# Optimization experiments

Measured on AMD Instinct MI355X. Metric: run time of the kernel, lower is better.

Reference implementation:

```python
import jax, jax.numpy as jnp
import numpy as np

B = 2048


def _maxpool2(x):
    return jax.lax.reduce_window(x, -jnp.inf, jax.lax.max,
                                 (1, 1, 2, 2), (1, 1, 2, 2), 'VALID')


def setup_inputs() -> dict:
    key = jax.random.key(0)
    ks = jax.random.split(key, 7)
    return {
        'x': jax.random.normal(ks[0], (B, 3, 32, 32), dtype=jnp.float32),
        'conv_w': jax.random.normal(ks[1], (45, 1, 5, 5), dtype=jnp.float32),
        'conv_b': jax.random.normal(ks[2], (45,), dtype=jnp.float32) * 0.1,
        'tree_w': jax.random.normal(ks[3], (1, 16, 15, 3, 7, 7, 2, 2), dtype=jnp.float32),
        'tree_b': jax.random.normal(ks[4], (1, 16, 3, 7), dtype=jnp.float32),
        'fc_w': jax.random.normal(ks[5], (10, 336), dtype=jnp.float32),
        'fc_b': jax.random.normal(ks[6], (10,), dtype=jnp.float32) * 0.1,
    }


def reference(x, conv_w, conv_b, tree_w, tree_b, fc_w, fc_b):
    # grouped conv: in=3, groups=3, out=45, kernel 5x5, VALID -> (B,45,28,28)
    out = jax.lax.conv_general_dilated(
        x, conv_w, window_strides=(1, 1), padding='VALID',
        dimension_numbers=('NCHW', 'OIHW', 'NCHW'), feature_group_count=3)
    out = jax.nn.sigmoid(out + conv_b[None, :, None, None])
    out = _maxpool2(out)  # (B,45,14,14)
    b = out.shape[0]
    # unfold((2,2),stride=2) + the torch reshape/transpose chain is equivalent to:
    # (B,45,14,14) -> (b, g=3, m=15, i=7, ki=2, j=7, kj=2) -> (b,m,g,i,j,ki,kj)
    xt = out.reshape(b, 3, 15, 7, 2, 7, 2).transpose(0, 2, 1, 3, 5, 4, 6)
    # TreeLayer: elementwise mul with weights (16,m,g,i,j,ki,kj) then sum over m,j,ki,kj
    t = jnp.einsum('bmgijkl,fmgijkl->bfgi', xt, tree_w[0]) + tree_b  # (B,16,3,7)
    t = jax.nn.sigmoid(t)
    return t.reshape(b, 16 * 3 * 7) @ fc_w.T + fc_b  # (B,10)
```

## Files before the change

kernel.cpp:

```cpp
#include <hip/hip_runtime.h>
#include <hip/hip_fp16.h>

#define BATCH 2048
#define NPREP 95

typedef _Float16 f16x8 __attribute__((ext_vector_type(8)));
typedef float f32x4 __attribute__((ext_vector_type(4)));

__device__ __forceinline__ float sigmoidf(float v) {
    return 1.0f / (1.0f + __expf(-v));
}

#define WS_W3B  0
#define WS_FCW  301056
#define WS_PS   322560
#define PS_G_STRIDE (7u * 2048u * 448u)

__global__ __launch_bounds__(256, 4) void kA_conv_prep(
    const float* __restrict__ x,
    const float* __restrict__ conv_w,
    const float* __restrict__ conv_b,
    const float* __restrict__ tree_w,
    const float* __restrict__ fc_w,
    ushort* __restrict__ W3B,
    float* __restrict__ FCW,
    ushort* __restrict__ ps3)
{
    __shared__ __align__(16) ushort xsc[3 * 4656];
    const int tid = threadIdx.x;

    if (blockIdx.x < NPREP) {
        int pidx = blockIdx.x * 256 + tid;
        if (pidx < 18816) {
            int gi = pidx / 896;
            int rem = pidx - gi * 896;
            int c = rem >> 6, lane2 = rem & 63;
            int f = lane2 & 15, qq = lane2 >> 4;
            int g = gi / 7, i = gi - g * 7;
            ushort h[8];
            #pragma unroll
            for (int u = 0; u < 8; u++) {
                int k = c * 32 + qq * 8 + u;
                int tt = k >> 6;
                int q2 = (k >> 4) & 3;
                int nn = k & 15;
                int u27 = tt * 4 + q2;
                int ki = u27 / 14;
                int pw = u27 - ki * 14;
                int j = pw >> 1, kj = pw & 1;
                float v = 0.f;
                if (nn < 15)
                    v = tree_w[(size_t)f * 8820 + nn * 588 + g * 196 + i * 28
                               + j * 4 + ki * 2 + kj];
                h[u] = __half_as_ushort(__float2half(v));
            }
            *(uint4*)(W3B + (size_t)pidx * 8) = *(uint4*)h;
        } else if (pidx < 24192) {
            int j = pidx - 18816;
            int f = j & 15, o = (j >> 4) & 15, gi = j >> 8;
            FCW[j] = (o < 10) ? fc_w[o * 336 + f * 21 + gi] : 0.f;
        }
        return;
    }

    const int img  = blockIdx.x - NPREP;
    const int lane = tid & 63;
    const int n    = lane & 15;
    const int q    = lane >> 4;
    const int wave = tid >> 6;

    const float4* xg = (const float4*)(x + (size_t)img * 3072);
    #pragma unroll
    for (int it = 0; it < 3; it++) {
        int idx = tid + it * 256;
        float4 v = xg[idx];
        int flat = idx * 4;
        int row = flat >> 5;
        int g = row >> 5, r = row & 31;
        int col = flat & 31;
        __half2 a = __float22half2_rn(make_float2(v.x, v.y));
        __half2 b = __float22half2_rn(make_float2(v.z, v.w));
        uint2 pk;
        pk.x = *(unsigned int*)&a;
        pk.y = *(unsigned int*)&b;
        *(uint2*)(xsc + g * 4656 + r * 36 + col) = pk;
    }
    if (tid < 96) {
        int g = tid >> 5, r = tid & 31;
        *(uint2*)(xsc + g * 4656 + r * 36 + 32) = make_uint2(0u, 0u);
    }

    f16x8 B1g[3], B2g[3];
    float biasg[3];
    #pragma unroll
    for (int g = 0; g < 3; g++) {
        f16x8 b1 = {0, 0, 0, 0, 0, 0, 0, 0};
        f16x8 b2 = {0, 0, 0, 0, 0, 0, 0, 0};
        float bb = 0.f;
        if (n < 15) {
            const float* wrow = conv_w + (g * 15 + n) * 25;
            #pragma unroll
            for (int u = 0; u < 5; u++) b1[u] = (_Float16)wrow[q * 5 + u];
            if (q == 0) {
                #pragma unroll
                for (int u = 0; u < 5; u++) b2[u] = (_Float16)wrow[20 + u];
            }
            bb = conv_b[g * 15 + n];
        }
        B1g[g] = b1; B2g[g] = b2; biasg[g] = bb;
    }
    __syncthreads();

    for (int t = tid; t < 2592; t += 256) {
        int gg = t / 864;
        int rem = t - gg * 864;
        int s = rem / 288 + 1;
        int rem2 = rem - (s - 1) * 288;
        int row = rem2 / 9, g4 = rem2 - row * 9;
        ushort* base = xsc + gg * 4656;
        ushort* dst = base + s * 1164 + row * 36 + g4 * 4;
        if (g4 == 8) { *(uint2*)dst = make_uint2(0u, 0u); continue; }
        uint2 lo = *(const uint2*)(base + row * 36 + g4 * 4);
        uint2 hi = *(const uint2*)(base + row * 36 + g4 * 4 + 4);
        unsigned int w0 = lo.x, w1 = lo.y, w2 = hi.x, w3 = hi.y;
        unsigned int o0, o1;
        if (s == 1)      { o0 = (w0 >> 16) | (w1 << 16); o1 = (w1 >> 16) | (w2 << 16); }
        else if (s == 2) { o0 = w1;                      o1 = w2; }
        else             { o0 = (w1 >> 16) | (w2 << 16); o1 = (w2 >> 16) | (w3 << 16); }
        *(uint2*)dst = make_uint2(o0, o1);
    }

    const int dr = (n >> 1) & 1, dc = n & 1, n4 = n >> 2;
    const int a2c = 144 - q * 36;
    int aoff[13], sv[13];
    #pragma unroll
    for (int it = 0; it < 13; it++) {
        int t = wave + it * 4;
        if (t < 49) {
            int pb = t * 4 + n4;
            int ph = pb / 14, pw = pb - ph * 14;
            int r = 2 * ph + dr, c = 2 * pw + dc;
            int s = c & 3;
            aoff[it] = s * 1164 + (r + q) * 36 + (c - s);
            int i = t / 7, tt = t - i * 7;
            sv[it] = (i * 2048 + img) * 448 + tt * 64 + lane;
        } else { aoff[it] = 0; sv[it] = 0; }
    }
    __syncthreads();

    #pragma unroll
    for (int g = 0; g < 3; g++) {
        const ushort* xb = xsc + g * 4656;
        const f16x8 B1 = B1g[g], B2 = B2g[g];
        const float bias = biasg[g];
        ushort* psg = ps3 + (size_t)g * PS_G_STRIDE;
        #pragma unroll
        for (int it = 0; it < 13; it++) {
            int t = wave + it * 4;
            if (t < 49) {
                const ushort* pA = xb + aoff[it];
                union { struct { uint2 a, b; } u; f16x8 v; } A1, A2;
                A1.u.a = *(const uint2*)pA;
                A1.u.b = *(const uint2*)(pA + 4);
                A2.u.a = *(const uint2*)(pA + a2c);
                A2.u.b = *(const uint2*)(pA + a2c + 4);
                f32x4 d = {0.f, 0.f, 0.f, 0.f};
                d = __builtin_amdgcn_mfma_f32_16x16x32_f16(A1.v, B1, d, 0, 0, 0);
                d = __builtin_amdgcn_mfma_f32_16x16x32_f16(A2.v, B2, d, 0, 0, 0);
                float mx = fmaxf(fmaxf(d[0], d[1]), fmaxf(d[2], d[3]));
                float val = (n < 15) ? sigmoidf(mx + bias) : 0.f;
                psg[sv[it]] = __half_as_ushort(__float2half(val));
            }
        }
    }
}

__global__ __launch_bounds__(128, 3) void kBC_tree_fc(
    const ushort* __restrict__ ps3,
    const ushort* __restrict__ W3B,
    const float* __restrict__ tree_b,
    const float* __restrict__ FCW,
    const float* __restrict__ fc_b,
    float* __restrict__ out)
{
    __shared__ __align__(16) ushort im[32 * 456];
    __shared__ __align__(16) ushort tsl[32 * 16];

    const int btile = blockIdx.x;
    const int gi    = blockIdx.y;
    const int img0  = btile * 32;
    const int tid   = threadIdx.x;
    const int lane  = tid & 63;
    const int n     = lane & 15;
    const int q     = lane >> 4;
    const int wave  = tid >> 6;

    const uint4* src = (const uint4*)(ps3 + ((size_t)gi * 2048 + img0) * 448);
    #pragma unroll
    for (int it = 0; it < 14; it++) {
        int t = tid + it * 128;
        int img = t / 56;
        int o = t - img * 56;
        *(uint4*)(im + img * 456 + o * 8) = src[t];
    }

    const f16x8* Wbase = (const f16x8*)W3B + (size_t)gi * 896;
    f16x8 B[14];
    #pragma unroll
    for (int c = 0; c < 14; c++) B[c] = Wbase[c * 64 + lane];
    __syncthreads();

    f32x4 D = {0.f, 0.f, 0.f, 0.f};
    const ushort* arow = im + (wave * 16 + n) * 456;
    #pragma unroll
    for (int c = 0; c < 14; c++) {
        f16x8 Af = *(const f16x8*)(arow + c * 32 + q * 8);
        D = __builtin_amdgcn_mfma_f32_16x16x32_f16(Af, B[c], D, 0, 0, 0);
    }

    float bias = tree_b[n * 21 + gi];
    #pragma unroll
    for (int r = 0; r < 4; r++) {
        int imgL = wave * 16 + q * 4 + r;
        tsl[imgL * 16 + n] = __half_as_ushort(__float2half(sigmoidf(D[r] + bias)));
    }
    __syncthreads();

    const float4* Wfc = (const float4*)(FCW + gi * 256);
    for (int t = tid; t < 320; t += 128) {
        int img = t / 10, o = t - (t / 10) * 10;
        const uint4* tp = (const uint4*)(tsl + img * 16);
        uint4 t0 = tp[0], t1 = tp[1];
        const __half2* h = (const __half2*)&t0;
        const __half2* h2 = (const __half2*)&t1;
        float4 w0 = Wfc[o * 4], w1 = Wfc[o * 4 + 1];
        float4 w2 = Wfc[o * 4 + 2], w3 = Wfc[o * 4 + 3];
        float acc = (gi == 0) ? fc_b[o] : 0.f;
        float2 p;
        p = __half22float2(h[0]);  acc = fmaf(p.x, w0.x, acc); acc = fmaf(p.y, w0.y, acc);
        p = __half22float2(h[1]);  acc = fmaf(p.x, w0.z, acc); acc = fmaf(p.y, w0.w, acc);
        p = __half22float2(h[2]);  acc = fmaf(p.x, w1.x, acc); acc = fmaf(p.y, w1.y, acc);
        p = __half22float2(h[3]);  acc = fmaf(p.x, w1.z, acc); acc = fmaf(p.y, w1.w, acc);
        p = __half22float2(h2[0]); acc = fmaf(p.x, w2.x, acc); acc = fmaf(p.y, w2.y, acc);
        p = __half22float2(h2[1]); acc = fmaf(p.x, w2.z, acc); acc = fmaf(p.y, w2.w, acc);
        p = __half22float2(h2[2]); acc = fmaf(p.x, w3.x, acc); acc = fmaf(p.y, w3.y, acc);
        p = __half22float2(h2[3]); acc = fmaf(p.x, w3.z, acc); acc = fmaf(p.y, w3.w, acc);
#if defined(__HIP_PLATFORM_AMD__)
        unsafeAtomicAdd(out + (size_t)(img0 + img) * 10 + o, acc);
#else
        atomicAdd(out + (size_t)(img0 + img) * 10 + o, acc);
#endif
    }
}

extern "C" void kernel_launch(void* const* d_in, const int* in_sizes, int n_in,
                              void* d_out, int out_size, void* d_ws, size_t ws_size,
                              hipStream_t stream) {
    const float* x      = (const float*)d_in[0];
    const float* conv_w = (const float*)d_in[1];
    const float* conv_b = (const float*)d_in[2];
    const float* tree_w = (const float*)d_in[3];
    const float* tree_b = (const float*)d_in[4];
    const float* fc_w   = (const float*)d_in[5];
    const float* fc_b   = (const float*)d_in[6];
    float* out = (float*)d_out;

    ushort* W3B = (ushort*)((char*)d_ws + WS_W3B);
    float*  FCW = (float*)((char*)d_ws + WS_FCW);
    ushort* ps3 = (ushort*)((char*)d_ws + WS_PS);

    hipMemsetAsync(out, 0, (size_t)BATCH * 10 * sizeof(float), stream);
    kA_conv_prep<<<BATCH + NPREP, 256, 0, stream>>>(x, conv_w, conv_b, tree_w,
                                                    fc_w, W3B, FCW, ps3);
    kBC_tree_fc<<<dim3(64, 21), 128, 0, stream>>>(ps3, W3B, tree_b, FCW, fc_b, out);
}
```

Before: 120.9 us.

## Split conv kernel work per (image pair, group) to raise occupancy

The conv stage is re-partitioned so each block handles one channel group for two images, instead of all three groups for one image. This cuts LDS per block from three image planes to two and raises the launch-bounds occupancy target from 4 to 8 blocks per CU, so more blocks are resident and the grid is larger. The 49-tile loop is restructured into 12 uniform iterations plus a wave-0 tail to drop the per-iteration bounds check. The trade-off is loading fewer conv weights per block and coarser per-block work, with a possible register-pressure risk under the tighter occupancy bound.

```diff
diff --git a/kernel.cpp b/kernel.cpp
--- a/kernel.cpp
+++ b/kernel.cpp
@@ -16,7 +16,7 @@
 #define WS_PS   322560
 #define PS_G_STRIDE (7u * 2048u * 448u)
 
-__global__ __launch_bounds__(256, 4) void kA_conv_prep(
+__global__ __launch_bounds__(256, 8) void kA_conv_prep(
     const float* __restrict__ x,
     const float* __restrict__ conv_w,
     const float* __restrict__ conv_b,
@@ -26,7 +26,7 @@
     float* __restrict__ FCW,
     ushort* __restrict__ ps3)
 {
-    __shared__ __align__(16) ushort xsc[3 * 4656];
+    __shared__ __align__(16) ushort xsc[2 * 4656];
     const int tid = threadIdx.x;
 
     if (blockIdx.x < NPREP) {
@@ -63,61 +63,53 @@
         return;
     }
 
-    const int img  = blockIdx.x - NPREP;
+    const int blk2 = blockIdx.x - NPREP;
+    const int pair = blk2 / 3;
+    const int g    = blk2 - pair * 3;
+    const int img0 = pair * 2;
     const int lane = tid & 63;
     const int n    = lane & 15;
     const int q    = lane >> 4;
     const int wave = tid >> 6;
 
-    const float4* xg = (const float4*)(x + (size_t)img * 3072);
-    #pragma unroll
-    for (int it = 0; it < 3; it++) {
-        int idx = tid + it * 256;
-        float4 v = xg[idx];
-        int flat = idx * 4;
-        int row = flat >> 5;
-        int g = row >> 5, r = row & 31;
-        int col = flat & 31;
+    #pragma unroll
+    for (int im2 = 0; im2 < 2; im2++) {
+        float4 v = ((const float4*)(x + (size_t)(img0 + im2) * 3072 + g * 1024))[tid];
+        int row = tid >> 3, col = (tid & 7) * 4;
         __half2 a = __float22half2_rn(make_float2(v.x, v.y));
         __half2 b = __float22half2_rn(make_float2(v.z, v.w));
         uint2 pk;
         pk.x = *(unsigned int*)&a;
         pk.y = *(unsigned int*)&b;
-        *(uint2*)(xsc + g * 4656 + r * 36 + col) = pk;
-    }
-    if (tid < 96) {
-        int g = tid >> 5, r = tid & 31;
-        *(uint2*)(xsc + g * 4656 + r * 36 + 32) = make_uint2(0u, 0u);
-    }
-
-    f16x8 B1g[3], B2g[3];
-    float biasg[3];
-    #pragma unroll
-    for (int g = 0; g < 3; g++) {
-        f16x8 b1 = {0, 0, 0, 0, 0, 0, 0, 0};
-        f16x8 b2 = {0, 0, 0, 0, 0, 0, 0, 0};
-        float bb = 0.f;
-        if (n < 15) {
-            const float* wrow = conv_w + (g * 15 + n) * 25;
+        *(uint2*)(xsc + im2 * 4656 + row * 36 + col) = pk;
+    }
+    if (tid < 64) {
+        int im2 = tid >> 5, r = tid & 31;
+        *(uint2*)(xsc + im2 * 4656 + r * 36 + 32) = make_uint2(0u, 0u);
+    }
+
+    f16x8 B1 = {0, 0, 0, 0, 0, 0, 0, 0};
+    f16x8 B2 = {0, 0, 0, 0, 0, 0, 0, 0};
+    float bias = 0.f;
+    if (n < 15) {
+        const float* wrow = conv_w + (g * 15 + n) * 25;
+        #pragma unroll
+        for (int u = 0; u < 5; u++) B1[u] = (_Float16)wrow[q * 5 + u];
+        if (q == 0) {
             #pragma unroll
-            for (int u = 0; u < 5; u++) b1[u] = (_Float16)wrow[q * 5 + u];
-            if (q == 0) {
-                #pragma unroll
-                for (int u = 0; u < 5; u++) b2[u] = (_Float16)wrow[20 + u];
-            }
-            bb = conv_b[g * 15 + n];
-        }
-        B1g[g] = b1; B2g[g] = b2; biasg[g] = bb;
-    }
-    __syncthreads();
-
-    for (int t = tid; t < 2592; t += 256) {
-        int gg = t / 864;
-        int rem = t - gg * 864;
+            for (int u = 0; u < 5; u++) B2[u] = (_Float16)wrow[20 + u];
+        }
+        bias = conv_b[g * 15 + n];
+    }
+    __syncthreads();
+
+    for (int t = tid; t < 1728; t += 256) {
+        int im2 = t / 864;
+        int rem = t - im2 * 864;
         int s = rem / 288 + 1;
         int rem2 = rem - (s - 1) * 288;
         int row = rem2 / 9, g4 = rem2 - row * 9;
-        ushort* base = xsc + gg * 4656;
+        ushort* base = xsc + im2 * 4656;
         ushort* dst = base + s * 1164 + row * 36 + g4 * 4;
         if (g4 == 8) { *(uint2*)dst = make_uint2(0u, 0u); continue; }
         uint2 lo = *(const uint2*)(base + row * 36 + g4 * 4);
@@ -132,45 +124,53 @@
 
     const int dr = (n >> 1) & 1, dc = n & 1, n4 = n >> 2;
     const int a2c = 144 - q * 36;
-    int aoff[13], sv[13];
+    int aoff[13], svr[13];
     #pragma unroll
     for (int it = 0; it < 13; it++) {
         int t = wave + it * 4;
-        if (t < 49) {
-            int pb = t * 4 + n4;
-            int ph = pb / 14, pw = pb - ph * 14;
-            int r = 2 * ph + dr, c = 2 * pw + dc;
-            int s = c & 3;
-            aoff[it] = s * 1164 + (r + q) * 36 + (c - s);
-            int i = t / 7, tt = t - i * 7;
-            sv[it] = (i * 2048 + img) * 448 + tt * 64 + lane;
-        } else { aoff[it] = 0; sv[it] = 0; }
-    }
-    __syncthreads();
-
-    #pragma unroll
-    for (int g = 0; g < 3; g++) {
-        const ushort* xb = xsc + g * 4656;
-        const f16x8 B1 = B1g[g], B2 = B2g[g];
-        const float bias = biasg[g];
-        ushort* psg = ps3 + (size_t)g * PS_G_STRIDE;
+        int pb = t * 4 + n4;
+        int ph = pb / 14, pw = pb - ph * 14;
+        int r = 2 * ph + dr, c = 2 * pw + dc;
+        int s = c & 3;
+        aoff[it] = s * 1164 + (r + q) * 36 + (c - s);
+        int i = t / 7, tt = t - i * 7;
+        svr[it] = i * (2048 * 448) + tt * 64 + lane;
+    }
+    __syncthreads();
+
+    ushort* psg = ps3 + (size_t)g * PS_G_STRIDE;
+    #pragma unroll
+    for (int im2 = 0; im2 < 2; im2++) {
+        const ushort* xb = xsc + im2 * 4656;
+        const int sb = (img0 + im2) * 448;
         #pragma unroll
-        for (int it = 0; it < 13; it++) {
-            int t = wave + it * 4;
-            if (t < 49) {
-                const ushort* pA = xb + aoff[it];
-                union { struct { uint2 a, b; } u; f16x8 v; } A1, A2;
-                A1.u.a = *(const uint2*)pA;
-                A1.u.b = *(const uint2*)(pA + 4);
-                A2.u.a = *(const uint2*)(pA + a2c);
-                A2.u.b = *(const uint2*)(pA + a2c + 4);
-                f32x4 d = {0.f, 0.f, 0.f, 0.f};
-                d = __builtin_amdgcn_mfma_f32_16x16x32_f16(A1.v, B1, d, 0, 0, 0);
-                d = __builtin_amdgcn_mfma_f32_16x16x32_f16(A2.v, B2, d, 0, 0, 0);
-                float mx = fmaxf(fmaxf(d[0], d[1]), fmaxf(d[2], d[3]));
-                float val = (n < 15) ? sigmoidf(mx + bias) : 0.f;
-                psg[sv[it]] = __half_as_ushort(__float2half(val));
-            }
+        for (int it = 0; it < 12; it++) {
+            const ushort* pA = xb + aoff[it];
+            union { struct { uint2 a, b; } u; f16x8 v; } A1, A2;
+            A1.u.a = *(const uint2*)pA;
+            A1.u.b = *(const uint2*)(pA + 4);
+            A2.u.a = *(const uint2*)(pA + a2c);
+            A2.u.b = *(const uint2*)(pA + a2c + 4);
+            f32x4 d = {0.f, 0.f, 0.f, 0.f};
+            d = __builtin_amdgcn_mfma_f32_16x16x32_f16(A1.v, B1, d, 0, 0, 0);
+            d = __builtin_amdgcn_mfma_f32_16x16x32_f16(A2.v, B2, d, 0, 0, 0);
+            float mx = fmaxf(fmaxf(d[0], d[1]), fmaxf(d[2], d[3]));
+            float val = (n < 15) ? sigmoidf(mx + bias) : 0.f;
+            psg[sb + svr[it]] = __half_as_ushort(__float2half(val));
+        }
+        if (wave == 0) {
+            const ushort* pA = xb + aoff[12];
+            union { struct { uint2 a, b; } u; f16x8 v; } A1, A2;
+            A1.u.a = *(const uint2*)pA;
+            A1.u.b = *(const uint2*)(pA + 4);
+            A2.u.a = *(const uint2*)(pA + a2c);
+            A2.u.b = *(const uint2*)(pA + a2c + 4);
+            f32x4 d = {0.f, 0.f, 0.f, 0.f};
+            d = __builtin_amdgcn_mfma_f32_16x16x32_f16(A1.v, B1, d, 0, 0, 0);
+            d = __builtin_amdgcn_mfma_f32_16x16x32_f16(A2.v, B2, d, 0, 0, 0);
+            float mx = fmaxf(fmaxf(d[0], d[1]), fmaxf(d[2], d[3]));
+            float val = (n < 15) ? sigmoidf(mx + bias) : 0.f;
+            psg[sb + svr[12]] = __half_as_ushort(__float2half(val));
         }
     }
 }
@@ -270,7 +270,7 @@
     ushort* ps3 = (ushort*)((char*)d_ws + WS_PS);
 
     hipMemsetAsync(out, 0, (size_t)BATCH * 10 * sizeof(float), stream);
-    kA_conv_prep<<<BATCH + NPREP, 256, 0, stream>>>(x, conv_w, conv_b, tree_w,
-                                                    fc_w, W3B, FCW, ps3);
+    kA_conv_prep<<<NPREP + 1024 * 3, 256, 0, stream>>>(x, conv_w, conv_b, tree_w,
+                                                       fc_w, W3B, FCW, ps3);
     kBC_tree_fc<<<dim3(64, 21), 128, 0, stream>>>(ps3, W3B, tree_b, FCW, fc_b, out);
 }
```

After: 123.2 us. No clear change (+1.9%).
